# Optimization experiments

Hardware: AMD Instinct MI355X
Metric: run time of the kernel (lower is better)

## Reference

```python
import jax, jax.numpy as jnp
import numpy as np
from jax import lax


def _nms(heat):
    # 3x3 max-pool, stride 1, SAME padding (torch pads with -inf for max pool)
    hmax = lax.reduce_window(heat, -jnp.inf, lax.max,
                             (1, 1, 3, 3), (1, 1, 1, 1), 'SAME')
    return jnp.where(hmax == heat, heat, jnp.zeros_like(heat))


def _decode(hmap, regs, w_h_, rot, K):
    B, C, H, W = hmap.shape
    heat = _nms(jax.nn.sigmoid(hmap))
    # stage 1: per-class top-k over the H*W spatial grid
    scores_flat = heat.reshape(B, C, H * W)
    topk_scores, topk_inds = lax.top_k(scores_flat, K)          # [B, C, K]
    topk_ys = (topk_inds // W).astype(heat.dtype)
    topk_xs = (topk_inds % W).astype(heat.dtype)
    # stage 2: top-k over all C*K candidates
    topk_score, topk_ind = lax.top_k(topk_scores.reshape(B, C * K), K)  # [B, K]
    clses = (topk_ind // K).astype(heat.dtype)                   # [B, K]
    inds = jnp.take_along_axis(topk_inds.reshape(B, C * K), topk_ind, axis=1)
    ys = jnp.take_along_axis(topk_ys.reshape(B, C * K), topk_ind, axis=1)
    xs = jnp.take_along_axis(topk_xs.reshape(B, C * K), topk_ind, axis=1)

    def gather_feat(feat):  # feat: [B, ch, H, W] -> [B, K, ch]
        ch = feat.shape[1]
        f = feat.transpose(0, 2, 3, 1).reshape(B, H * W, ch)
        return jnp.take_along_axis(f, inds[:, :, None], axis=1)

    regs_g = gather_feat(regs)   # [B, K, 2]
    wh_g = gather_feat(w_h_)     # [B, K, 2]
    rot_g = gather_feat(rot)     # [B, K, 1]
    xs = xs[:, :, None] + regs_g[:, :, 0:1]
    ys = ys[:, :, None] + regs_g[:, :, 1:2]
    # detections: [x, y, w, h, rot, score, cls] -> [B, K, 7]
    return jnp.concatenate(
        [xs, ys, wh_g, rot_g, topk_score[:, :, None], clses[:, :, None]], axis=2)


def setup_inputs() -> dict:
    key = jax.random.key(0)
    k1, k2, k3, k4 = jax.random.split(key, 4)
    B, C, H, W = 1, 80, 512, 512
    return {
        'hmap': jax.random.normal(k1, (B, C, H, W), dtype=jnp.float32),
        'regs': jax.random.normal(k2, (B, 2, H, W), dtype=jnp.float32),
        'w_h_': jax.random.uniform(k3, (B, 2, H, W), dtype=jnp.float32) * 64.0,
        'rot': jax.random.normal(k4, (B, 1, H, W), dtype=jnp.float32),
        'K': 100,
    }


def reference(hmap, regs, w_h_, rot, K):
    return _decode(hmap, regs, w_h_, rot, K)
```

## Files before the change

kernel.cpp:

```cpp
#include <hip/hip_runtime.h>
#include <cstdint>

#define HH 512
#define WW 512
#define HWSZ (HH * WW)
#define TILE_H 8
#define NSEG 128
#define SEGPAD 16
#define SEGCAP 256
#define FCAP 4096
#define T0F 3.75f
#define BINBASE 8248u
#define NVB 1024

__device__ __forceinline__ float sigmoid_f(float x) {
    return 1.0f / (1.0f + expf(-x));
}

__device__ __forceinline__ uint32_t vbin(uint32_t key) {
    uint32_t b = (key >> 17) - BINBASE;
    return b > (NVB - 1) ? (NVB - 1) : b;
}

__global__ __launch_bounds__(64) void main_pass(const float* __restrict__ hmap,
                                                int nTiles,
                                                uint32_t* __restrict__ segCount,
                                                uint2* __restrict__ cand) {
    int tile = blockIdx.x;
    if (tile >= nTiles) return;
    const int lane = threadIdx.x;
    const int cls = tile >> 6;
    const int ty = tile & 63;
    const int y0 = ty * TILE_H;
    const float* base = hmap + (size_t)cls * HWSZ;
    const int xA = lane * 4;
    const int xB = 256 + lane * 4;
    const int seg = tile & (NSEG - 1);
    const float NEG = -__builtin_inff();

    float4 A0, A1, A2, A3, B0, B1, B2, B3;
    int rm1 = (y0 > 0) ? y0 - 1 : 0;
    A0 = *(const float4*)(base + rm1 * WW + xA);
    B0 = *(const float4*)(base + rm1 * WW + xB);
    A1 = *(const float4*)(base + y0 * WW + xA);
    B1 = *(const float4*)(base + y0 * WW + xB);
    A2 = *(const float4*)(base + (y0 + 1) * WW + xA);
    B2 = *(const float4*)(base + (y0 + 1) * WW + xB);
    A3 = A2; B3 = B2;

    #pragma unroll
    for (int r = 0; r < TILE_H; ++r) {
        if (r < TILE_H - 1) {
            int j = y0 + 2 + r;
            int jc = (j < HH) ? j : HH - 1;
            A3 = *(const float4*)(base + jc * WW + xA);
            B3 = *(const float4*)(base + jc * WW + xB);
        }
        float cA = fmaxf(fmaxf(A1.x, A1.y), fmaxf(A1.z, A1.w));
        float cB = fmaxf(fmaxf(B1.x, B1.y), fmaxf(B1.z, B1.w));
        if (__any(fmaxf(cA, cB) >= T0F)) {
            float4 vA, vB;
            vA.x = fmaxf(fmaxf(A0.x, A1.x), A2.x);
            vA.y = fmaxf(fmaxf(A0.y, A1.y), A2.y);
            vA.z = fmaxf(fmaxf(A0.z, A1.z), A2.z);
            vA.w = fmaxf(fmaxf(A0.w, A1.w), A2.w);
            vB.x = fmaxf(fmaxf(B0.x, B1.x), B2.x);
            vB.y = fmaxf(fmaxf(B0.y, B1.y), B2.y);
            vB.z = fmaxf(fmaxf(B0.z, B1.z), B2.z);
            vB.w = fmaxf(fmaxf(B0.w, B1.w), B2.w);
            float vAl = __shfl_up(vA.w, 1);
            float vAr = __shfl_down(vA.x, 1);
            float vBl = __shfl_up(vB.w, 1);
            float vBr = __shfl_down(vB.x, 1);
            float seamR = __shfl(vB.x, 0);
            float seamL = __shfl(vA.w, 63);
            if (lane == 0)  { vAl = NEG; vBl = seamL; }
            if (lane == 63) { vAr = seamR; vBr = NEG; }
            float mA0 = fmaxf(fmaxf(vAl, vA.x), vA.y);
            float mA1 = fmaxf(fmaxf(vA.x, vA.y), vA.z);
            float mA2 = fmaxf(fmaxf(vA.y, vA.z), vA.w);
            float mA3 = fmaxf(fmaxf(vA.z, vA.w), vAr);
            float mB0 = fmaxf(fmaxf(vBl, vB.x), vB.y);
            float mB1 = fmaxf(fmaxf(vB.x, vB.y), vB.z);
            float mB2 = fmaxf(fmaxf(vB.y, vB.z), vB.w);
            float mB3 = fmaxf(fmaxf(vB.z, vB.w), vBr);

            int row = y0 + r;
            auto testc = [&](float c, float m, int col) {
                if (c >= T0F && (m <= c + 0.7f || c > 14.0f)) {
                    float s = sigmoid_f(c), sm = sigmoid_f(m);
                    if (s == sm) {
                        uint32_t slot = atomicAdd(&segCount[seg * SEGPAD], 1u);
                        if (slot < SEGCAP)
                            cand[seg * SEGCAP + slot] = make_uint2(
                                __float_as_uint(c),
                                (uint32_t)(cls * HWSZ + row * WW + col));
                    }
                }
            };
            testc(A1.x, mA0, xA + 0); testc(A1.y, mA1, xA + 1);
            testc(A1.z, mA2, xA + 2); testc(A1.w, mA3, xA + 3);
            testc(B1.x, mB0, xB + 0); testc(B1.y, mB1, xB + 1);
            testc(B1.z, mB2, xB + 2); testc(B1.w, mB3, xB + 3);
        }
        A0 = A1; A1 = A2; A2 = A3; B0 = B1; B1 = B2; B2 = B3;
    }
}

__global__ __launch_bounds__(256) void finalize_kernel(
        const uint2* __restrict__ cand, const uint32_t* __restrict__ segCount,
        const int* __restrict__ Kp, const float* __restrict__ hmap,
        const float* __restrict__ regs, const float* __restrict__ wh,
        const float* __restrict__ rot, int total, float* __restrict__ out) {
    __shared__ uint2 flat[FCAP];
    __shared__ uint32_t vhist[NVB];
    __shared__ uint32_t sOff[NSEG + 1];
    __shared__ uint32_t cnts[NSEG];
    __shared__ uint32_t chunkSum[128];
    __shared__ int sFlag, sN, sKept, sThr;

    int t = threadIdx.x;
    int K = *Kp;
    if (t == 0) { sFlag = 0; sKept = 0; }
    for (int i = t; i < NVB; i += 256) vhist[i] = 0;
    if (t < NSEG) {
        uint32_t c = segCount[t * SEGPAD];
        if (c > SEGCAP) { sFlag = 1; c = SEGCAP; }
        cnts[t] = c;
    }
    __syncthreads();
    if (t == 0) {
        uint32_t o = 0;
        for (int s = 0; s < NSEG; ++s) { sOff[s] = o; o += cnts[s]; }
        sOff[NSEG] = o;
        sN = (int)o;
        if ((int)o < K || o > FCAP) sFlag = 1;
    }
    __syncthreads();
    int flag = sFlag;
    int n;

    if (!flag) {
        n = sN;
        for (int k0 = t * 4; k0 < n; k0 += 1024) {
            uint2 r[4]; int kk[4]; int nv = 0;
            #pragma unroll
            for (int u = 0; u < 4; ++u) {
                int k = k0 + u;
                if (k < n) {
                    int lo = 0, hi = NSEG;
                    while (hi - lo > 1) {
                        int mid = (lo + hi) >> 1;
                        if (sOff[mid] <= (uint32_t)k) lo = mid; else hi = mid;
                    }
                    r[u] = cand[lo * SEGCAP + (k - (int)sOff[lo])];
                    kk[u] = k; nv = u + 1;
                }
            }
            #pragma unroll
            for (int u = 0; u < 4; ++u)
                if (u < nv) flat[kk[u]] = r[u];
        }
        __syncthreads();
    } else {
        for (int gid = t; gid < total; gid += 256) {
            float ctr = hmap[gid];
            if (ctr < T0F) continue;
            int pos = gid & (HWSZ - 1);
            int y = pos >> 9, x = pos & (WW - 1);
            const float* bse = hmap + (gid - pos);
            float m = ctr;
            int yl = y > 0 ? y - 1 : 0, yh = y < HH - 1 ? y + 1 : HH - 1;
            int xl = x > 0 ? x - 1 : 0, xh = x < WW - 1 ? x + 1 : WW - 1;
            for (int yy = yl; yy <= yh; ++yy)
                for (int xx = xl; xx <= xh; ++xx)
                    m = fmaxf(m, bse[yy * WW + xx]);
            float s = sigmoid_f(ctr), sm = sigmoid_f(m);
            if (s == sm) {
                int slot = atomicAdd(&sKept, 1);
                if (slot < FCAP) flat[slot] = make_uint2(__float_as_uint(ctr), (uint32_t)gid);
            }
        }
        __syncthreads();
        n = min(sKept, FCAP);
        __syncthreads();
        if (t == 0) sKept = 0;
    }

    for (int k = t; k < n; k += 256) atomicAdd(&vhist[vbin(flat[k].x)], 1u);
    __syncthreads();
    if (t < 128) {
        uint32_t s = 0;
        for (int i = 0; i < 8; ++i) s += vhist[t * 8 + i];
        chunkSum[t] = s;
    }
    __syncthreads();
    if (t == 0) {
        uint32_t cum = 0; int thr = 0; bool fnd = false;
        for (int c = 127; c >= 0 && !fnd; --c) {
            if (cum + chunkSum[c] >= (uint32_t)K) {
                for (int b = c * 8 + 7; b >= c * 8; --b) {
                    cum += vhist[b];
                    if (cum >= (uint32_t)K) { thr = b; fnd = true; break; }
                }
            } else cum += chunkSum[c];
        }
        sThr = fnd ? (thr > 0 ? thr - 1 : 0) : 0;
    }
    __syncthreads();
    uint32_t thrM1 = (uint32_t)sThr;

    for (int bse = 0; bse < n; bse += 256) {
        uint2 rec; bool keep = false;
        int k = bse + t;
        if (k < n) { rec = flat[k]; keep = vbin(rec.x) >= thrM1; }
        __syncthreads();
        if (keep) {
            float s = sigmoid_f(__uint_as_float(rec.x));
            int slot = atomicAdd(&sKept, 1);
            flat[slot] = make_uint2(__float_as_uint(s), rec.y);
        }
        __syncthreads();
    }
    int m = sKept;
    if (m > FCAP) m = FCAP;

    for (int i = t; i < m; i += 256) {
        uint2 me = flat[i];
        int rank = 0;
        for (int j = 0; j < m; ++j) {
            uint2 o = flat[j];
            rank += (int)((o.x > me.x) || (o.x == me.x && o.y < me.y));
        }
        if (rank < K) {
            int gid = (int)me.y;
            int cls = gid >> 18;
            int pos = gid & (HWSZ - 1);
            float yf = (float)(pos >> 9);
            float xf = (float)(pos & (WW - 1));
            float* o7 = out + rank * 7;
            o7[0] = xf + regs[pos];
            o7[1] = yf + regs[HWSZ + pos];
            o7[2] = wh[pos];
            o7[3] = wh[HWSZ + pos];
            o7[4] = rot[pos];
            o7[5] = __uint_as_float(me.x);
            o7[6] = (float)cls;
        }
    }
}

extern "C" void kernel_launch(void* const* d_in, const int* in_sizes, int n_in,
                              void* d_out, int out_size, void* d_ws, size_t ws_size,
                              hipStream_t stream) {
    const float* hmap = (const float*)d_in[0];
    const float* regs = (const float*)d_in[1];
    const float* wh   = (const float*)d_in[2];
    const float* rot  = (const float*)d_in[3];
    const int*   Kp   = (const int*)d_in[4];
    float* out = (float*)d_out;

    int total = in_sizes[0];
    int nTiles = (total / HWSZ) * (HH / TILE_H);

    uint32_t* ws = (uint32_t*)d_ws;
    uint32_t* segCount = ws;
    uint2* cand = (uint2*)(ws + NSEG * SEGPAD);

    hipMemsetAsync(d_ws, 0, (size_t)NSEG * SEGPAD * sizeof(uint32_t), stream);
    main_pass<<<nTiles, 64, 0, stream>>>(hmap, nTiles, segCount, cand);
    finalize_kernel<<<1, 256, 0, stream>>>(cand, segCount, Kp, hmap, regs, wh, rot,
                                           total, out);
}
```

Measured before the change: 153.1 us.

## Use per-tile candidate slots with ballot compaction instead of global atomics

Replaces the shared-segment atomic candidate buffer with per-tile slots filled through wave ballot and popcount prefix, so the memset and atomics go away. Main pass now runs four wavefronts per block and loads all eight rows up front. Halo rows are fetched only when an edge row is hot. Finalize does a per-thread prefix over tile counts and copies each tile's candidates directly, dropping the binary search. The per-tile cap of 16 may overflow more often and force the slow fallback path.

```diff
diff --git a/kernel.cpp b/kernel.cpp
--- a/kernel.cpp
+++ b/kernel.cpp
@@ -5,9 +5,7 @@
 #define WW 512
 #define HWSZ (HH * WW)
 #define TILE_H 8
-#define NSEG 128
-#define SEGPAD 16
-#define SEGCAP 256
+#define TCAP 16
 #define FCAP 4096
 #define T0F 3.75f
 #define BINBASE 8248u
@@ -22,52 +20,68 @@
     return b > (NVB - 1) ? (NVB - 1) : b;
 }
 
-__global__ __launch_bounds__(64) void main_pass(const float* __restrict__ hmap,
-                                                int nTiles,
-                                                uint32_t* __restrict__ segCount,
-                                                uint2* __restrict__ cand) {
-    int tile = blockIdx.x;
+__global__ __launch_bounds__(256) void main_pass(const float* __restrict__ hmap,
+                                                 int nTiles,
+                                                 uint32_t* __restrict__ counts,
+                                                 uint2* __restrict__ cand) {
+    const int lane = threadIdx.x & 63;
+    const int tile = blockIdx.x * 4 + (threadIdx.x >> 6);
     if (tile >= nTiles) return;
-    const int lane = threadIdx.x;
     const int cls = tile >> 6;
     const int ty = tile & 63;
     const int y0 = ty * TILE_H;
     const float* base = hmap + (size_t)cls * HWSZ;
     const int xA = lane * 4;
     const int xB = 256 + lane * 4;
-    const int seg = tile & (NSEG - 1);
     const float NEG = -__builtin_inff();
 
-    float4 A0, A1, A2, A3, B0, B1, B2, B3;
-    int rm1 = (y0 > 0) ? y0 - 1 : 0;
-    A0 = *(const float4*)(base + rm1 * WW + xA);
-    B0 = *(const float4*)(base + rm1 * WW + xB);
-    A1 = *(const float4*)(base + y0 * WW + xA);
-    B1 = *(const float4*)(base + y0 * WW + xB);
-    A2 = *(const float4*)(base + (y0 + 1) * WW + xA);
-    B2 = *(const float4*)(base + (y0 + 1) * WW + xB);
-    A3 = A2; B3 = B2;
-
+    float4 RA[8], RB[8];
     #pragma unroll
-    for (int r = 0; r < TILE_H; ++r) {
-        if (r < TILE_H - 1) {
-            int j = y0 + 2 + r;
-            int jc = (j < HH) ? j : HH - 1;
-            A3 = *(const float4*)(base + jc * WW + xA);
-            B3 = *(const float4*)(base + jc * WW + xB);
-        }
-        float cA = fmaxf(fmaxf(A1.x, A1.y), fmaxf(A1.z, A1.w));
-        float cB = fmaxf(fmaxf(B1.x, B1.y), fmaxf(B1.z, B1.w));
-        if (__any(fmaxf(cA, cB) >= T0F)) {
+    for (int r = 0; r < 8; ++r) {
+        RA[r] = *(const float4*)(base + (y0 + r) * WW + xA);
+        RB[r] = *(const float4*)(base + (y0 + r) * WW + xB);
+    }
+
+    uint32_t cnt = 0;
+
+    bool hot[8]; bool anyhot = false;
+    #pragma unroll
+    for (int r = 0; r < 8; ++r) {
+        float rmA = fmaxf(fmaxf(RA[r].x, RA[r].y), fmaxf(RA[r].z, RA[r].w));
+        float rmB = fmaxf(fmaxf(RB[r].x, RB[r].y), fmaxf(RB[r].z, RB[r].w));
+        hot[r] = __any(fmaxf(rmA, rmB) >= T0F);
+        anyhot |= hot[r];
+    }
+
+    if (anyhot) {
+        float4 TA = RA[0], TB = RB[0], BA = RA[7], BB = RB[7];
+        if (hot[0]) {
+            int rt = (y0 > 0) ? y0 - 1 : 0;
+            TA = *(const float4*)(base + rt * WW + xA);
+            TB = *(const float4*)(base + rt * WW + xB);
+        }
+        if (hot[7]) {
+            int rb = (y0 + 8 < HH) ? y0 + 8 : HH - 1;
+            BA = *(const float4*)(base + rb * WW + xA);
+            BB = *(const float4*)(base + rb * WW + xB);
+        }
+
+        #pragma unroll
+        for (int r = 0; r < 8; ++r) {
+            if (!hot[r]) continue;
+            float4 Am = (r == 0) ? TA : RA[r - 1];
+            float4 Ap = (r == 7) ? BA : RA[r + 1];
+            float4 Bm = (r == 0) ? TB : RB[r - 1];
+            float4 Bp = (r == 7) ? BB : RB[r + 1];
             float4 vA, vB;
-            vA.x = fmaxf(fmaxf(A0.x, A1.x), A2.x);
-            vA.y = fmaxf(fmaxf(A0.y, A1.y), A2.y);
-            vA.z = fmaxf(fmaxf(A0.z, A1.z), A2.z);
-            vA.w = fmaxf(fmaxf(A0.w, A1.w), A2.w);
-            vB.x = fmaxf(fmaxf(B0.x, B1.x), B2.x);
-            vB.y = fmaxf(fmaxf(B0.y, B1.y), B2.y);
-            vB.z = fmaxf(fmaxf(B0.z, B1.z), B2.z);
-            vB.w = fmaxf(fmaxf(B0.w, B1.w), B2.w);
+            vA.x = fmaxf(fmaxf(Am.x, RA[r].x), Ap.x);
+            vA.y = fmaxf(fmaxf(Am.y, RA[r].y), Ap.y);
+            vA.z = fmaxf(fmaxf(Am.z, RA[r].z), Ap.z);
+            vA.w = fmaxf(fmaxf(Am.w, RA[r].w), Ap.w);
+            vB.x = fmaxf(fmaxf(Bm.x, RB[r].x), Bp.x);
+            vB.y = fmaxf(fmaxf(Bm.y, RB[r].y), Bp.y);
+            vB.z = fmaxf(fmaxf(Bm.z, RB[r].z), Bp.z);
+            vB.w = fmaxf(fmaxf(Bm.w, RB[r].w), Bp.w);
             float vAl = __shfl_up(vA.w, 1);
             float vAr = __shfl_down(vA.x, 1);
             float vBl = __shfl_up(vB.w, 1);
@@ -76,46 +90,49 @@
             float seamL = __shfl(vA.w, 63);
             if (lane == 0)  { vAl = NEG; vBl = seamL; }
             if (lane == 63) { vAr = seamR; vBr = NEG; }
-            float mA0 = fmaxf(fmaxf(vAl, vA.x), vA.y);
-            float mA1 = fmaxf(fmaxf(vA.x, vA.y), vA.z);
-            float mA2 = fmaxf(fmaxf(vA.y, vA.z), vA.w);
-            float mA3 = fmaxf(fmaxf(vA.z, vA.w), vAr);
-            float mB0 = fmaxf(fmaxf(vBl, vB.x), vB.y);
-            float mB1 = fmaxf(fmaxf(vB.x, vB.y), vB.z);
-            float mB2 = fmaxf(fmaxf(vB.y, vB.z), vB.w);
-            float mB3 = fmaxf(fmaxf(vB.z, vB.w), vBr);
-
+            float mm[8];
+            mm[0] = fmaxf(fmaxf(vAl, vA.x), vA.y);
+            mm[1] = fmaxf(fmaxf(vA.x, vA.y), vA.z);
+            mm[2] = fmaxf(fmaxf(vA.y, vA.z), vA.w);
+            mm[3] = fmaxf(fmaxf(vA.z, vA.w), vAr);
+            mm[4] = fmaxf(fmaxf(vBl, vB.x), vB.y);
+            mm[5] = fmaxf(fmaxf(vB.x, vB.y), vB.z);
+            mm[6] = fmaxf(fmaxf(vB.y, vB.z), vB.w);
+            mm[7] = fmaxf(fmaxf(vB.z, vB.w), vBr);
+            float cc[8] = { RA[r].x, RA[r].y, RA[r].z, RA[r].w,
+                            RB[r].x, RB[r].y, RB[r].z, RB[r].w };
             int row = y0 + r;
-            auto testc = [&](float c, float m, int col) {
-                if (c >= T0F && (m <= c + 0.7f || c > 14.0f)) {
-                    float s = sigmoid_f(c), sm = sigmoid_f(m);
-                    if (s == sm) {
-                        uint32_t slot = atomicAdd(&segCount[seg * SEGPAD], 1u);
-                        if (slot < SEGCAP)
-                            cand[seg * SEGCAP + slot] = make_uint2(
-                                __float_as_uint(c),
-                                (uint32_t)(cls * HWSZ + row * WW + col));
-                    }
+            #pragma unroll
+            for (int p = 0; p < 8; ++p) {
+                float c = cc[p], m = mm[p];
+                bool pass = false;
+                if (c >= T0F && (m <= c + 0.7f || c > 14.0f))
+                    pass = (sigmoid_f(c) == sigmoid_f(m));
+                unsigned long long mask = __ballot(pass);
+                if (pass) {
+                    uint32_t slot = cnt +
+                        (uint32_t)__popcll(mask & ((1ULL << lane) - 1ULL));
+                    int col = (p < 4) ? (xA + p) : (xB + p - 4);
+                    if (slot < TCAP)
+                        cand[(size_t)tile * TCAP + slot] = make_uint2(
+                            __float_as_uint(c),
+                            (uint32_t)(cls * HWSZ + row * WW + col));
                 }
-            };
-            testc(A1.x, mA0, xA + 0); testc(A1.y, mA1, xA + 1);
-            testc(A1.z, mA2, xA + 2); testc(A1.w, mA3, xA + 3);
-            testc(B1.x, mB0, xB + 0); testc(B1.y, mB1, xB + 1);
-            testc(B1.z, mB2, xB + 2); testc(B1.w, mB3, xB + 3);
-        }
-        A0 = A1; A1 = A2; A2 = A3; B0 = B1; B1 = B2; B2 = B3;
-    }
+                cnt += (uint32_t)__popcll(mask);
+            }
+        }
+    }
+    if (lane == 0) counts[tile] = cnt;
 }
 
 __global__ __launch_bounds__(256) void finalize_kernel(
-        const uint2* __restrict__ cand, const uint32_t* __restrict__ segCount,
-        const int* __restrict__ Kp, const float* __restrict__ hmap,
+        const uint2* __restrict__ cand, const uint32_t* __restrict__ counts,
+        int nTiles, const int* __restrict__ Kp, const float* __restrict__ hmap,
         const float* __restrict__ regs, const float* __restrict__ wh,
         const float* __restrict__ rot, int total, float* __restrict__ out) {
     __shared__ uint2 flat[FCAP];
     __shared__ uint32_t vhist[NVB];
-    __shared__ uint32_t sOff[NSEG + 1];
-    __shared__ uint32_t cnts[NSEG];
+    __shared__ uint32_t tsum[256];
     __shared__ uint32_t chunkSum[128];
     __shared__ int sFlag, sN, sKept, sThr;
 
@@ -123,16 +140,23 @@
     int K = *Kp;
     if (t == 0) { sFlag = 0; sKept = 0; }
     for (int i = t; i < NVB; i += 256) vhist[i] = 0;
-    if (t < NSEG) {
-        uint32_t c = segCount[t * SEGPAD];
-        if (c > SEGCAP) { sFlag = 1; c = SEGCAP; }
-        cnts[t] = c;
-    }
+    __syncthreads();
+
+    int TPT = (nTiles + 255) / 256;
+    uint32_t mysum = 0;
+    for (int i = 0; i < TPT; ++i) {
+        int tid = i * 256 + t;
+        if (tid < nTiles) {
+            uint32_t c = counts[tid];
+            if (c > TCAP) { sFlag = 1; c = TCAP; }
+            mysum += c;
+        }
+    }
+    tsum[t] = mysum;
     __syncthreads();
     if (t == 0) {
         uint32_t o = 0;
-        for (int s = 0; s < NSEG; ++s) { sOff[s] = o; o += cnts[s]; }
-        sOff[NSEG] = o;
+        for (int i = 0; i < 256; ++i) { uint32_t c = tsum[i]; tsum[i] = o; o += c; }
         sN = (int)o;
         if ((int)o < K || o > FCAP) sFlag = 1;
     }
@@ -142,24 +166,14 @@
 
     if (!flag) {
         n = sN;
-        for (int k0 = t * 4; k0 < n; k0 += 1024) {
-            uint2 r[4]; int kk[4]; int nv = 0;
-            #pragma unroll
-            for (int u = 0; u < 4; ++u) {
-                int k = k0 + u;
-                if (k < n) {
-                    int lo = 0, hi = NSEG;
-                    while (hi - lo > 1) {
-                        int mid = (lo + hi) >> 1;
-                        if (sOff[mid] <= (uint32_t)k) lo = mid; else hi = mid;
-                    }
-                    r[u] = cand[lo * SEGCAP + (k - (int)sOff[lo])];
-                    kk[u] = k; nv = u + 1;
-                }
+        uint32_t off = tsum[t];
+        for (int i = 0; i < TPT; ++i) {
+            int tid = i * 256 + t;
+            if (tid < nTiles) {
+                uint32_t c = counts[tid];
+                for (uint32_t j = 0; j < c; ++j)
+                    flat[off++] = cand[(size_t)tid * TCAP + j];
             }
-            #pragma unroll
-            for (int u = 0; u < 4; ++u)
-                if (u < nv) flat[kk[u]] = r[u];
         }
         __syncthreads();
     } else {
@@ -262,13 +276,13 @@
 
     int total = in_sizes[0];
     int nTiles = (total / HWSZ) * (HH / TILE_H);
+    int nBlocks = (nTiles + 3) / 4;
 
     uint32_t* ws = (uint32_t*)d_ws;
-    uint32_t* segCount = ws;
-    uint2* cand = (uint2*)(ws + NSEG * SEGPAD);
-
-    hipMemsetAsync(d_ws, 0, (size_t)NSEG * SEGPAD * sizeof(uint32_t), stream);
-    main_pass<<<nTiles, 64, 0, stream>>>(hmap, nTiles, segCount, cand);
-    finalize_kernel<<<1, 256, 0, stream>>>(cand, segCount, Kp, hmap, regs, wh, rot,
-                                           total, out);
-}
+    uint32_t* counts = ws;
+    uint2* cand = (uint2*)(ws + nTiles);
+
+    main_pass<<<nBlocks, 256, 0, stream>>>(hmap, nTiles, counts, cand);
+    finalize_kernel<<<1, 256, 0, stream>>>(cand, counts, nTiles, Kp, hmap,
+                                           regs, wh, rot, total, out);
+}
```

New measurement: 175.7 us. +14.7%, slower.
